# Performance work log

Measured on AMD Instinct MI355X. Metric: run time of the kernel, lower is better.

The kernel has to match this reference:

```python
import jax, jax.numpy as jnp
import numpy as np

D_IN = 2048
NUM_HEADS = 32
NUM_KV = 8
HEAD_DIM = 64
V_HEAD_DIM = 64
SEQ = 2048
BATCH = 1
EPS = 1e-6
NEG = -1e30


def setup_inputs() -> dict:
    key = jax.random.key(0)
    ks = jax.random.split(key, 10)
    x = jax.random.normal(ks[0], (BATCH, SEQ, D_IN), dtype=jnp.float32)
    # causal mask: True = masked out (upper triangle above diagonal)
    mask = jnp.triu(jnp.ones((SEQ, SEQ), dtype=jnp.bool_), k=1)
    # RoPE tables
    inv_freq = 1.0 / (10000.0 ** (jnp.arange(0, HEAD_DIM, 2, dtype=jnp.float32) / HEAD_DIM))
    t = jnp.arange(SEQ, dtype=jnp.float32)
    freqs = jnp.outer(t, inv_freq)  # (S, hd/2)
    emb = jnp.concatenate([freqs, freqs], axis=-1)  # (S, hd)
    cos = jnp.cos(emb)
    sin = jnp.sin(emb)
    scale = 0.02
    wq = jax.random.normal(ks[1], (D_IN, NUM_HEADS * HEAD_DIM), dtype=jnp.float32) * scale
    wk = jax.random.normal(ks[2], (D_IN, NUM_KV * HEAD_DIM), dtype=jnp.float32) * scale
    wv = jax.random.normal(ks[3], (D_IN, NUM_KV * V_HEAD_DIM), dtype=jnp.float32) * scale
    wo = jax.random.normal(ks[4], (NUM_HEADS * V_HEAD_DIM, D_IN), dtype=jnp.float32) * scale
    q_norm_w = jnp.ones((HEAD_DIM,), dtype=jnp.float32)
    k_norm_w = jnp.ones((HEAD_DIM,), dtype=jnp.float32)
    sink = jax.random.normal(ks[5], (NUM_HEADS,), dtype=jnp.float32) * 0.02
    return {"x": x, "mask": mask, "cos": cos, "sin": sin, "wq": wq, "wk": wk,
            "wv": wv, "wo": wo, "q_norm_w": q_norm_w, "k_norm_w": k_norm_w, "sink": sink}


def _rmsnorm(x, w):
    var = jnp.mean(jnp.square(x), axis=-1, keepdims=True)
    return x * jax.lax.rsqrt(var + EPS) * w


def _rope(x, cos, sin):
    # x: (b, h, s, d); cos/sin: (s, d)
    d = x.shape[-1]
    x1, x2 = x[..., : d // 2], x[..., d // 2:]
    rot = jnp.concatenate([-x2, x1], axis=-1)
    return x * cos[None, None] + rot * sin[None, None]


def reference(x, mask, cos, sin, wq, wk, wv, wo, q_norm_w, k_norm_w, sink):
    b, s, _ = x.shape
    rep = NUM_HEADS // NUM_KV
    q = (x @ wq).reshape(b, s, NUM_HEADS, HEAD_DIM).transpose(0, 2, 1, 3)
    k = (x @ wk).reshape(b, s, NUM_KV, HEAD_DIM).transpose(0, 2, 1, 3)
    v = (x @ wv).reshape(b, s, NUM_KV, V_HEAD_DIM).transpose(0, 2, 1, 3)
    q = _rope(_rmsnorm(q, q_norm_w), cos, sin)
    k = _rope(_rmsnorm(k, k_norm_w), cos, sin)
    k = jnp.repeat(k, rep, axis=1)  # (b, H, s, hd)
    v = jnp.repeat(v, rep, axis=1)  # (b, H, s, vd)
    scores = jnp.einsum('bhqd,bhkd->bhqk', q, k) * (HEAD_DIM ** -0.5)
    scores = jnp.where(mask[:s, :s], NEG, scores)
    # append learnable sink logit per head
    sink_col = jnp.broadcast_to(sink.reshape(1, NUM_HEADS, 1, 1), (b, NUM_HEADS, s, 1))
    scores = jnp.concatenate([scores, sink_col], axis=-1)
    weights = jax.nn.softmax(scores, axis=-1)[..., :-1]  # drop sink column
    out = jnp.einsum('bhqk,bhkd->bhqd', weights, v)
    out = out.transpose(0, 2, 1, 3).reshape(b, s, NUM_HEADS * V_HEAD_DIM)
    return out @ wo
```

## Files before the change

### kernel.cpp

```cpp
#include <hip/hip_runtime.h>

typedef unsigned short u16;
typedef __bf16 bf16;
typedef float f32x4 __attribute__((ext_vector_type(4)));
typedef bf16 bf16x8 __attribute__((ext_vector_type(8)));
typedef short s16x4 __attribute__((ext_vector_type(4)));
typedef u16 u16x4 __attribute__((ext_vector_type(4)));
typedef u16 u16x8 __attribute__((ext_vector_type(8)));

#define SEQ 2048
#define LOG2E 1.4426950408889634f

__device__ __forceinline__ u16 f2bf(float f) {
    return __builtin_bit_cast(u16, (bf16)f);
}
__device__ __forceinline__ float bf2f(u16 u) {
    unsigned int w = ((unsigned int)u) << 16;
    return __builtin_bit_cast(float, w);
}

__global__ __launch_bounds__(256) void cast_bf16_k(const float* __restrict__ in,
                                                   u16* __restrict__ out, int n4) {
    int i = blockIdx.x * 256 + threadIdx.x;
    int stride = gridDim.x * 256;
    for (; i < n4; i += stride) {
        float4 v = reinterpret_cast<const float4*>(in)[i];
        u16x4 o;
        o[0] = f2bf(v.x); o[1] = f2bf(v.y); o[2] = f2bf(v.z); o[3] = f2bf(v.w);
        reinterpret_cast<u16x4*>(out)[i] = o;
    }
}

__global__ __launch_bounds__(256) void transpose_all_k(const float* __restrict__ wq,
                                                       const float* __restrict__ wk,
                                                       const float* __restrict__ wv,
                                                       const float* __restrict__ wo,
                                                       u16* __restrict__ wqkvt,
                                                       u16* __restrict__ wot) {
    __shared__ float t[64][65];
    int b = blockIdx.x;
    const float* src;
    u16* dst;
    int C, bx, by;
    if (b < 1024)      { src = wq; dst = wqkvt;                         C = 2048; bx = b & 31; by = b >> 5; }
    else if (b < 1280) { b -= 1024; src = wk; dst = wqkvt + (size_t)2048 * 2048; C = 512;  bx = b & 7;  by = b >> 3; }
    else if (b < 1536) { b -= 1280; src = wv; dst = wqkvt + (size_t)2560 * 2048; C = 512;  bx = b & 7;  by = b >> 3; }
    else               { b -= 1536; src = wo; dst = wot;                C = 2048; bx = b & 31; by = b >> 5; }
    int c0 = bx * 64, r0 = by * 64;
    int tx = threadIdx.x & 63, ty = threadIdx.x >> 6;
#pragma unroll
    for (int i = 0; i < 16; ++i) {
        int r = ty + i * 4;
        t[r][tx] = src[(size_t)(r0 + r) * C + c0 + tx];
    }
    __syncthreads();
#pragma unroll
    for (int i = 0; i < 16; ++i) {
        int c = ty + i * 4;
        dst[(size_t)(c0 + c) * 2048 + r0 + tx] = f2bf(t[tx][c]);
    }
}

__global__ __launch_bounds__(256) void gemm_bt_dbuf_k(const u16* __restrict__ A,
                                                      const u16* __restrict__ Bt,
                                                      u16* __restrict__ Cp,
                                                      int M, int N, int K) {
    __shared__ __align__(16) u16 As[2][128 * 32];
    __shared__ __align__(16) u16 Bs[2][128 * 32];
    int tid = threadIdx.x;
    int wave = tid >> 6, lane = tid & 63;

    unsigned nx = gridDim.x, ny = gridDim.y;
    unsigned nwg = nx * ny * gridDim.z;
    unsigned id = blockIdx.x + nx * (blockIdx.y + ny * blockIdx.z);
    unsigned qq = nwg >> 3;
    unsigned swz = (id & 7) * qq + (id >> 3);
    unsigned bxw = swz % nx;
    unsigned rem = swz / nx;
    unsigned byw = rem % ny;
    unsigned bzw = rem / ny;
    int bm = byw * 128, bn = bxw * 128;
    int z = bzw;

    int kslice = K / gridDim.z;
    int kt0 = z * kslice, ktend = kt0 + kslice;
    int wm = (wave >> 1) * 64, wn = (wave & 1) * 64;
    int g = lane >> 4, cidx = lane & 15;
    f32x4 acc[4][4] = {};

    int srow = lane >> 2;
    int skol = ((lane & 3) ^ ((srow >> 1) & 3)) * 8;
    int sl8 = (g ^ ((cidx >> 1) & 3)) * 8;

#define STAGE(buf, kt)                                                                \
    {                                                                                 \
        _Pragma("unroll")                                                             \
        for (int j = 0; j < 2; ++j) {                                                 \
            const u16* gpa = A + (size_t)(bm + (wave * 2 + j) * 16 + srow) * K + (kt) + skol; \
            __builtin_amdgcn_global_load_lds(                                         \
                (__attribute__((address_space(1))) void*)gpa,                         \
                (__attribute__((address_space(3))) void*)&As[buf][(wave * 2 + j) * 512], \
                16, 0, 0);                                                            \
        }                                                                             \
        _Pragma("unroll")                                                             \
        for (int j = 0; j < 2; ++j) {                                                 \
            const u16* gpb = Bt + (size_t)(bn + (wave * 2 + j) * 16 + srow) * K + (kt) + skol; \
            __builtin_amdgcn_global_load_lds(                                         \
                (__attribute__((address_space(1))) void*)gpb,                         \
                (__attribute__((address_space(3))) void*)&Bs[buf][(wave * 2 + j) * 512], \
                16, 0, 0);                                                            \
        }                                                                             \
    }

    STAGE(0, kt0);
    asm volatile("s_waitcnt vmcnt(0)" ::: "memory");
    __syncthreads();

    int cur = 0;
#pragma unroll 1
    for (int kt = kt0; kt < ktend; kt += 32) {
        if (kt + 32 < ktend) STAGE(cur ^ 1, kt + 32);

        bf16x8 af[4], bfr[4];
#pragma unroll
        for (int mi = 0; mi < 4; ++mi)
            af[mi] = *reinterpret_cast<const bf16x8*>(&As[cur][(wm + mi * 16 + cidx) * 32 + sl8]);
#pragma unroll
        for (int ni = 0; ni < 4; ++ni)
            bfr[ni] = *reinterpret_cast<const bf16x8*>(&Bs[cur][(wn + ni * 16 + cidx) * 32 + sl8]);
#pragma unroll
        for (int mi = 0; mi < 4; ++mi)
#pragma unroll
            for (int ni = 0; ni < 4; ++ni)
                acc[mi][ni] = __builtin_amdgcn_mfma_f32_16x16x32_bf16(af[mi], bfr[ni], acc[mi][ni], 0, 0, 0);

        asm volatile("s_waitcnt vmcnt(0)" ::: "memory");
        __syncthreads();
        cur ^= 1;
    }
#undef STAGE

    u16* cbase = Cp + (size_t)z * M * N;
#pragma unroll
    for (int mi = 0; mi < 4; ++mi) {
#pragma unroll
        for (int r = 0; r < 4; ++r) {
            int row = bm + wm + mi * 16 + g * 4 + r;
            u16* cp = cbase + (size_t)row * N + bn + wn + cidx;
#pragma unroll
            for (int ni = 0; ni < 4; ++ni)
                cp[ni * 16] = f2bf(acc[mi][ni][r]);
        }
    }
}

__global__ __launch_bounds__(256) void sum2_f32_k(const u16* __restrict__ a,
                                                  const u16* __restrict__ b,
                                                  float* __restrict__ out, int n8) {
    int i = blockIdx.x * 256 + threadIdx.x;
    if (i >= n8) return;
    u16x8 va = reinterpret_cast<const u16x8*>(a)[i];
    u16x8 vb = reinterpret_cast<const u16x8*>(b)[i];
    f32x4 lo, hi;
#pragma unroll
    for (int j = 0; j < 4; ++j) {
        lo[j] = bf2f(va[j]) + bf2f(vb[j]);
        hi[j] = bf2f(va[4 + j]) + bf2f(vb[4 + j]);
    }
    reinterpret_cast<f32x4*>(out)[i * 2] = lo;
    reinterpret_cast<f32x4*>(out)[i * 2 + 1] = hi;
}

__global__ __launch_bounds__(256) void norm_rope_k(const u16* __restrict__ p0,
                                                   const u16* __restrict__ p1,
                                                   const float* __restrict__ cosb,
                                                   const float* __restrict__ sinb,
                                                   const float* __restrict__ qw,
                                                   const float* __restrict__ kw,
                                                   u16* __restrict__ qn,
                                                   u16* __restrict__ kfrag) {
    int idx = blockIdx.x * 4 + (threadIdx.x >> 6);
    int lane = threadIdx.x & 63;
    int s = idx / 40, hh = idx - s * 40;
    size_t off = (hh < 32) ? ((size_t)s * 3072 + hh * 64 + lane)
                           : ((size_t)s * 3072 + 2048 + (hh - 32) * 64 + lane);
    float val = bf2f(p0[off]) + bf2f(p1[off]);
    float ss = val * val;
#pragma unroll
    for (int mm = 32; mm; mm >>= 1) ss += __shfl_xor(ss, mm);
    float w = (hh < 32) ? qw[lane] : kw[lane];
    float xn = val * rsqrtf(ss * (1.f / 64.f) + 1e-6f) * w;
    float part = __shfl_xor(xn, 32);
    float rot = (lane < 32) ? -part : part;
    float o = xn * cosb[s * 64 + lane] + rot * sinb[s * 64 + lane];
    if (hh < 32) {
        qn[(size_t)s * 2048 + hh * 64 + lane] = f2bf(o * (0.125f * LOG2E));
    } else {
        int h8 = hh - 32;
        int k32 = s & 31;
        int p32 = ((k32 >> 2) & 1) * 16 + ((k32 >> 3) << 2) + (k32 & 3);
        int p = (s & ~31) + p32;
        kfrag[(((size_t)h8 * 128 + (p >> 4)) << 10) + (lane >> 3) * 128 + (p & 15) * 8 + (lane & 7)] = f2bf(o);
    }
}

__global__ __launch_bounds__(256) void v_frag_k(const u16* __restrict__ p0,
                                                const u16* __restrict__ p1,
                                                u16* __restrict__ vfrag) {
    __shared__ float t[64][65];
    int s0 = blockIdx.x * 64;
    int h = blockIdx.y;
    int tx = threadIdx.x & 63, ty = threadIdx.x >> 6;
#pragma unroll
    for (int i = 0; i < 16; ++i) {
        int r = ty + i * 4;
        size_t off = (size_t)(s0 + r) * 3072 + 2560 + h * 64 + tx;
        t[r][tx] = bf2f(p0[off]) + bf2f(p1[off]);
    }
    __syncthreads();
    int dt = threadIdx.x >> 6, g = (threadIdx.x >> 4) & 3, cc = threadIdx.x & 15;
#pragma unroll
    for (int kb = 0; kb < 2; ++kb) {
        u16x8 o;
#pragma unroll
        for (int i = 0; i < 8; ++i) o[i] = f2bf(t[kb * 32 + g * 8 + i][dt * 16 + cc]);
        *reinterpret_cast<u16x8*>(
            &vfrag[((size_t)h * 64 + (s0 >> 5) + kb) * 2048 + dt * 512 + (size_t)(threadIdx.x & 63) * 8]) = o;
    }
}

__global__ __launch_bounds__(64, 3) void attn_k(const u16* __restrict__ qn,
                                                const u16* __restrict__ kfrag,
                                                const u16* __restrict__ vfrag,
                                                u16* __restrict__ obuf,
                                                float* __restrict__ lbuf) {
    int h = blockIdx.x;
    int kvh = h >> 2;
    int lane = threadIdx.x;
    int item = 159 - blockIdx.y;
    int t, w;
    if (item < 16)      { t = item;                    w = 0; }
    else if (item < 48) { t = 16 + ((item - 16) >> 1); w = (item - 16) & 1; }
    else if (item < 96) { int r = item - 48; int q = r / 3; t = 32 + q; w = r - 3 * q; }
    else                { t = 48 + ((item - 96) >> 2); w = (item - 96) & 3; }

    int qA0 = t * 32;
    int qB0 = qA0 + 16;
    int kv0 = w * 512;
    int nkA = qA0 + 16, nkB = qB0 + 16;
    int kvend = (kv0 + 512 < nkB) ? (kv0 + 512) : nkB;

    int g = lane >> 4, cc = lane & 15;
    int qrowA = qA0 + cc, qrowB = qB0 + cc;

    const size_t qoffA = (size_t)qrowA * 2048 + h * 64;
    const size_t qoffB = (size_t)qrowB * 2048 + h * 64;
    bf16x8 qa0 = *reinterpret_cast<const bf16x8*>(&qn[qoffA + g * 8]);
    bf16x8 qa1 = *reinterpret_cast<const bf16x8*>(&qn[qoffA + 32 + g * 8]);
    bf16x8 qb0 = *reinterpret_cast<const bf16x8*>(&qn[qoffB + g * 8]);
    bf16x8 qb1 = *reinterpret_cast<const bf16x8*>(&qn[qoffB + 32 + g * 8]);

    float lA = 0.f, lB = 0.f;
    f32x4 oA[4] = {}, oB[4] = {};

    const u16* kbase = kfrag + (((size_t)kvh * 128) << 10) + lane * 8;
    const u16* vbase = vfrag + (size_t)kvh * 64 * 2048 + lane * 8;

#pragma unroll 1
    for (; kv0 < kvend; kv0 += 64) {
        bf16x8 kf0[4], kf1[4], vv[2][4];
#pragma unroll
        for (int sub = 0; sub < 4; ++sub) {
            const u16* kp = kbase + (size_t)((kv0 >> 4) + sub) * 1024;
            kf0[sub] = *reinterpret_cast<const bf16x8*>(kp);
            kf1[sub] = *reinterpret_cast<const bf16x8*>(kp + 512);
        }
#pragma unroll
        for (int sp = 0; sp < 2; ++sp)
#pragma unroll
            for (int dt = 0; dt < 4; ++dt)
                vv[sp][dt] = *reinterpret_cast<const bf16x8*>(
                    vbase + (size_t)((kv0 >> 5) + sp) * 2048 + dt * 512);

        bool doA = kv0 < nkA;

        if (doA) {
            f32x4 st[4];
            __builtin_amdgcn_s_setprio(1);
#pragma unroll
            for (int sub = 0; sub < 4; ++sub) {
                st[sub] = __builtin_amdgcn_mfma_f32_16x16x32_bf16(kf0[sub], qa0, (f32x4){0.f, 0.f, 0.f, 0.f}, 0, 0, 0);
                st[sub] = __builtin_amdgcn_mfma_f32_16x16x32_bf16(kf1[sub], qa1, st[sub], 0, 0, 0);
            }
            __builtin_amdgcn_s_setprio(0);
            if (kv0 + 64 > qA0) {
#pragma unroll
                for (int sub = 0; sub < 4; ++sub)
#pragma unroll
                    for (int r = 0; r < 4; ++r) {
                        int key = kv0 + (sub >> 1) * 32 + g * 8 + (sub & 1) * 4 + r;
                        if (key > qrowA) st[sub][r] = -1e30f;
                    }
            }
            u16x8 pb[2];
            float rs = 0.f;
#pragma unroll
            for (int sub = 0; sub < 4; ++sub)
#pragma unroll
                for (int r = 0; r < 4; ++r) {
                    float e = __builtin_amdgcn_exp2f(st[sub][r]);
                    rs += e;
                    pb[sub >> 1][(sub & 1) * 4 + r] = f2bf(e);
                }
            lA += rs;
            __builtin_amdgcn_s_setprio(1);
#pragma unroll
            for (int sp = 0; sp < 2; ++sp) {
                bf16x8 pbb = __builtin_bit_cast(bf16x8, pb[sp]);
#pragma unroll
                for (int dt = 0; dt < 4; ++dt)
                    oA[dt] = __builtin_amdgcn_mfma_f32_16x16x32_bf16(vv[sp][dt], pbb, oA[dt], 0, 0, 0);
            }
            __builtin_amdgcn_s_setprio(0);
        }

        {
            f32x4 st[4];
            __builtin_amdgcn_s_setprio(1);
#pragma unroll
            for (int sub = 0; sub < 4; ++sub) {
                st[sub] = __builtin_amdgcn_mfma_f32_16x16x32_bf16(kf0[sub], qb0, (f32x4){0.f, 0.f, 0.f, 0.f}, 0, 0, 0);
                st[sub] = __builtin_amdgcn_mfma_f32_16x16x32_bf16(kf1[sub], qb1, st[sub], 0, 0, 0);
            }
            __builtin_amdgcn_s_setprio(0);
            if (kv0 + 64 > qB0) {
#pragma unroll
                for (int sub = 0; sub < 4; ++sub)
#pragma unroll
                    for (int r = 0; r < 4; ++r) {
                        int key = kv0 + (sub >> 1) * 32 + g * 8 + (sub & 1) * 4 + r;
                        if (key > qrowB) st[sub][r] = -1e30f;
                    }
            }
            u16x8 pb[2];
            float rs = 0.f;
#pragma unroll
            for (int sub = 0; sub < 4; ++sub)
#pragma unroll
                for (int r = 0; r < 4; ++r) {
                    float e = __builtin_amdgcn_exp2f(st[sub][r]);
                    rs += e;
                    pb[sub >> 1][(sub & 1) * 4 + r] = f2bf(e);
                }
            lB += rs;
            __builtin_amdgcn_s_setprio(1);
#pragma unroll
            for (int sp = 0; sp < 2; ++sp) {
                bf16x8 pbb = __builtin_bit_cast(bf16x8, pb[sp]);
#pragma unroll
                for (int dt = 0; dt < 4; ++dt)
                    oB[dt] = __builtin_amdgcn_mfma_f32_16x16x32_bf16(vv[sp][dt], pbb, oB[dt], 0, 0, 0);
            }
            __builtin_amdgcn_s_setprio(0);
        }
    }

    lA += __shfl_xor(lA, 16);
    lA += __shfl_xor(lA, 32);
    lB += __shfl_xor(lB, 16);
    lB += __shfl_xor(lB, 32);
    size_t slotA = ((size_t)h * 160 + item) * 2;
    if (lane < 16) {
        lbuf[slotA * 16 + cc] = lA;
        lbuf[(slotA + 1) * 16 + cc] = lB;
    }
    u16* spA = obuf + slotA * 1024;
    u16* spB = obuf + (slotA + 1) * 1024;
#pragma unroll
    for (int dt = 0; dt < 4; ++dt) {
        u16x4 ovA, ovB;
#pragma unroll
        for (int r = 0; r < 4; ++r) {
            ovA[r] = f2bf(oA[dt][r]);
            ovB[r] = f2bf(oB[dt][r]);
        }
        *reinterpret_cast<u16x4*>(&spA[cc * 64 + dt * 16 + g * 4]) = ovA;
        *reinterpret_cast<u16x4*>(&spB[cc * 64 + dt * 16 + g * 4]) = ovB;
    }
}

__global__ __launch_bounds__(256) void merge_k(const u16* __restrict__ obuf,
                                               const float* __restrict__ lbuf,
                                               const float* __restrict__ sink,
                                               u16* __restrict__ attnb) {
    int row = blockIdx.x;
    int c = row >> 4, cc = row & 15;
    int t2 = c >> 1, half = c & 1;
    int nw = (t2 >> 4) + 1;
    int jb = (t2 < 16) ? t2
           : (t2 < 32) ? 16 + ((t2 - 16) << 1)
           : (t2 < 48) ? 48 + 3 * (t2 - 32)
                       : 96 + ((t2 - 48) << 2);
    int t = threadIdx.x;
    int h = t >> 3, col0 = (t & 7) * 8;

    float acc[8] = {};
    float lsum = __builtin_amdgcn_exp2f(sink[h] * LOG2E);
#pragma unroll 1
    for (int w = 0; w < nw; ++w) {
        size_t slot = ((size_t)h * 160 + jb + w) * 2 + half;
        lsum += lbuf[slot * 16 + cc];
        u16x8 v = *reinterpret_cast<const u16x8*>(&obuf[slot * 1024 + cc * 64 + col0]);
#pragma unroll
        for (int i = 0; i < 8; ++i) acc[i] += bf2f(v[i]);
    }
    float inv = 1.f / lsum;
    u16x8 ob;
#pragma unroll
    for (int i = 0; i < 8; ++i) ob[i] = f2bf(acc[i] * inv);
    *reinterpret_cast<u16x8*>(&attnb[(size_t)row * 2048 + h * 64 + col0]) = ob;
}

extern "C" void kernel_launch(void* const* d_in, const int* in_sizes, int n_in,
                              void* d_out, int out_size, void* d_ws, size_t ws_size,
                              hipStream_t stream) {
    const float* x    = (const float*)d_in[0];
    const float* cosb = (const float*)d_in[2];
    const float* sinb = (const float*)d_in[3];
    const float* wq   = (const float*)d_in[4];
    const float* wk   = (const float*)d_in[5];
    const float* wv   = (const float*)d_in[6];
    const float* wo   = (const float*)d_in[7];
    const float* qw   = (const float*)d_in[8];
    const float* kw   = (const float*)d_in[9];
    const float* sink = (const float*)d_in[10];
    float* out = (float*)d_out;

    char* ws = (char*)d_ws;
    size_t off = 0;
    auto alloc = [&](size_t bytes) {
        char* p = ws + off;
        off += (bytes + 255) & ~(size_t)255;
        return p;
    };
    u16*   xb    = (u16*)alloc((size_t)2048 * 2048 * 2);
    u16*   wqkvt = (u16*)alloc((size_t)3072 * 2048 * 2);
    u16*   wot   = (u16*)alloc((size_t)2048 * 2048 * 2);
    u16*   p0    = (u16*)alloc((size_t)2048 * 3072 * 2);
    u16*   p1    = (u16*)alloc((size_t)2048 * 3072 * 2);
    u16*   qnb   = (u16*)alloc((size_t)2048 * 2048 * 2);
    u16*   kfrag = (u16*)alloc((size_t)8 * 128 * 1024 * 2);
    u16*   vfrag = (u16*)alloc((size_t)8 * 64 * 2048 * 2);
    float* lbuf  = (float*)alloc((size_t)32 * 320 * 16 * 4);
    u16*   attnb = xb;
    u16*   obuf  = p0;
    u16*   o2p   = p0;

    cast_bf16_k<<<2048, 256, 0, stream>>>(x, xb, 2048 * 2048 / 4);
    transpose_all_k<<<2560, 256, 0, stream>>>(wq, wk, wv, wo, wqkvt, wot);

    gemm_bt_dbuf_k<<<dim3(24, 16, 2), 256, 0, stream>>>(xb, wqkvt, p0, 2048, 3072, 2048);
    norm_rope_k<<<20480, 256, 0, stream>>>(p0, p1, cosb, sinb, qw, kw, qnb, kfrag);
    v_frag_k<<<dim3(32, 8), 256, 0, stream>>>(p0, p1, vfrag);

    attn_k<<<dim3(32, 160), 64, 0, stream>>>(qnb, kfrag, vfrag, obuf, lbuf);
    merge_k<<<2048, 256, 0, stream>>>(obuf, lbuf, sink, attnb);

    gemm_bt_dbuf_k<<<dim3(16, 16, 2), 256, 0, stream>>>(attnb, wot, o2p, 2048, 2048, 2048);
    sum2_f32_k<<<2048, 256, 0, stream>>>(o2p, o2p + (size_t)2048 * 2048, out, 2048 * 2048 / 8);
}
```

Baseline: 140.7 us.

## Merge prep and post-GEMM kernels; restructure attention loop and raise occupancy

Combines the x cast and weight transposes into one prep kernel, and the norm/RoPE and V-fragment kernels into one post-GEMM kernel, removing two launches. In the attention kernel, V loads are deferred until after both score blocks are computed and the PV MFMAs for both query halves are interleaved. Launch bounds go from 3 to 4 waves per SIMD. The higher occupancy target lowers the per-thread register budget and could cause spills, and the fused kernels mix dissimilar block workloads.

```diff
diff --git a/kernel.cpp b/kernel.cpp
--- a/kernel.cpp
+++ b/kernel.cpp
@@ -19,33 +19,35 @@
     return __builtin_bit_cast(float, w);
 }
 
-__global__ __launch_bounds__(256) void cast_bf16_k(const float* __restrict__ in,
-                                                   u16* __restrict__ out, int n4) {
-    int i = blockIdx.x * 256 + threadIdx.x;
-    int stride = gridDim.x * 256;
-    for (; i < n4; i += stride) {
-        float4 v = reinterpret_cast<const float4*>(in)[i];
-        u16x4 o;
-        o[0] = f2bf(v.x); o[1] = f2bf(v.y); o[2] = f2bf(v.z); o[3] = f2bf(v.w);
-        reinterpret_cast<u16x4*>(out)[i] = o;
-    }
-}
-
-__global__ __launch_bounds__(256) void transpose_all_k(const float* __restrict__ wq,
-                                                       const float* __restrict__ wk,
-                                                       const float* __restrict__ wv,
-                                                       const float* __restrict__ wo,
-                                                       u16* __restrict__ wqkvt,
-                                                       u16* __restrict__ wot) {
+__global__ __launch_bounds__(256) void prep_k(const float* __restrict__ x,
+                                              const float* __restrict__ wq,
+                                              const float* __restrict__ wk,
+                                              const float* __restrict__ wv,
+                                              const float* __restrict__ wo,
+                                              u16* __restrict__ xb,
+                                              u16* __restrict__ wqkvt,
+                                              u16* __restrict__ wot) {
     __shared__ float t[64][65];
     int b = blockIdx.x;
+    if (b < 2048) {
+        int i = b * 256 + threadIdx.x;
+#pragma unroll
+        for (int it = 0; it < 2; ++it, i += 524288) {
+            float4 v = reinterpret_cast<const float4*>(x)[i];
+            u16x4 o;
+            o[0] = f2bf(v.x); o[1] = f2bf(v.y); o[2] = f2bf(v.z); o[3] = f2bf(v.w);
+            reinterpret_cast<u16x4*>(xb)[i] = o;
+        }
+        return;
+    }
+    b -= 2048;
     const float* src;
     u16* dst;
     int C, bx, by;
-    if (b < 1024)      { src = wq; dst = wqkvt;                         C = 2048; bx = b & 31; by = b >> 5; }
-    else if (b < 1280) { b -= 1024; src = wk; dst = wqkvt + (size_t)2048 * 2048; C = 512;  bx = b & 7;  by = b >> 3; }
-    else if (b < 1536) { b -= 1280; src = wv; dst = wqkvt + (size_t)2560 * 2048; C = 512;  bx = b & 7;  by = b >> 3; }
-    else               { b -= 1536; src = wo; dst = wot;                C = 2048; bx = b & 31; by = b >> 5; }
+    if (b < 1024)      { src = wq; dst = wqkvt;                          C = 2048; bx = b & 31; by = b >> 5; }
+    else if (b < 1280) { b -= 1024; src = wk; dst = wqkvt + (size_t)2048 * 2048; C = 512; bx = b & 7; by = b >> 3; }
+    else if (b < 1536) { b -= 1280; src = wv; dst = wqkvt + (size_t)2560 * 2048; C = 512; bx = b & 7; by = b >> 3; }
+    else               { b -= 1536; src = wo; dst = wot;                 C = 2048; bx = b & 31; by = b >> 5; }
     int c0 = bx * 64, r0 = by * 64;
     int tx = threadIdx.x & 63, ty = threadIdx.x >> 6;
 #pragma unroll
@@ -171,45 +173,45 @@
     reinterpret_cast<f32x4*>(out)[i * 2 + 1] = hi;
 }
 
-__global__ __launch_bounds__(256) void norm_rope_k(const u16* __restrict__ p0,
-                                                   const u16* __restrict__ p1,
-                                                   const float* __restrict__ cosb,
-                                                   const float* __restrict__ sinb,
-                                                   const float* __restrict__ qw,
-                                                   const float* __restrict__ kw,
-                                                   u16* __restrict__ qn,
-                                                   u16* __restrict__ kfrag) {
-    int idx = blockIdx.x * 4 + (threadIdx.x >> 6);
-    int lane = threadIdx.x & 63;
-    int s = idx / 40, hh = idx - s * 40;
-    size_t off = (hh < 32) ? ((size_t)s * 3072 + hh * 64 + lane)
-                           : ((size_t)s * 3072 + 2048 + (hh - 32) * 64 + lane);
-    float val = bf2f(p0[off]) + bf2f(p1[off]);
-    float ss = val * val;
-#pragma unroll
-    for (int mm = 32; mm; mm >>= 1) ss += __shfl_xor(ss, mm);
-    float w = (hh < 32) ? qw[lane] : kw[lane];
-    float xn = val * rsqrtf(ss * (1.f / 64.f) + 1e-6f) * w;
-    float part = __shfl_xor(xn, 32);
-    float rot = (lane < 32) ? -part : part;
-    float o = xn * cosb[s * 64 + lane] + rot * sinb[s * 64 + lane];
-    if (hh < 32) {
-        qn[(size_t)s * 2048 + hh * 64 + lane] = f2bf(o * (0.125f * LOG2E));
-    } else {
-        int h8 = hh - 32;
-        int k32 = s & 31;
-        int p32 = ((k32 >> 2) & 1) * 16 + ((k32 >> 3) << 2) + (k32 & 3);
-        int p = (s & ~31) + p32;
-        kfrag[(((size_t)h8 * 128 + (p >> 4)) << 10) + (lane >> 3) * 128 + (p & 15) * 8 + (lane & 7)] = f2bf(o);
-    }
-}
-
-__global__ __launch_bounds__(256) void v_frag_k(const u16* __restrict__ p0,
-                                                const u16* __restrict__ p1,
-                                                u16* __restrict__ vfrag) {
+__global__ __launch_bounds__(256) void postgemm_k(const u16* __restrict__ p0,
+                                                  const u16* __restrict__ p1,
+                                                  const float* __restrict__ cosb,
+                                                  const float* __restrict__ sinb,
+                                                  const float* __restrict__ qw,
+                                                  const float* __restrict__ kw,
+                                                  u16* __restrict__ qn,
+                                                  u16* __restrict__ kfrag,
+                                                  u16* __restrict__ vfrag) {
     __shared__ float t[64][65];
-    int s0 = blockIdx.x * 64;
-    int h = blockIdx.y;
+    int b = blockIdx.x;
+    if (b < 20480) {
+        int idx = b * 4 + (threadIdx.x >> 6);
+        int lane = threadIdx.x & 63;
+        int s = idx / 40, hh = idx - s * 40;
+        size_t off = (hh < 32) ? ((size_t)s * 3072 + hh * 64 + lane)
+                               : ((size_t)s * 3072 + 2048 + (hh - 32) * 64 + lane);
+        float val = bf2f(p0[off]) + bf2f(p1[off]);
+        float ss = val * val;
+#pragma unroll
+        for (int mm = 32; mm; mm >>= 1) ss += __shfl_xor(ss, mm);
+        float w = (hh < 32) ? qw[lane] : kw[lane];
+        float xn = val * rsqrtf(ss * (1.f / 64.f) + 1e-6f) * w;
+        float part = __shfl_xor(xn, 32);
+        float rot = (lane < 32) ? -part : part;
+        float o = xn * cosb[s * 64 + lane] + rot * sinb[s * 64 + lane];
+        if (hh < 32) {
+            qn[(size_t)s * 2048 + hh * 64 + lane] = f2bf(o * (0.125f * LOG2E));
+        } else {
+            int h8 = hh - 32;
+            int k32 = s & 31;
+            int p32 = ((k32 >> 2) & 1) * 16 + ((k32 >> 3) << 2) + (k32 & 3);
+            int p = (s & ~31) + p32;
+            kfrag[(((size_t)h8 * 128 + (p >> 4)) << 10) + (lane >> 3) * 128 + (p & 15) * 8 + (lane & 7)] = f2bf(o);
+        }
+        return;
+    }
+    int vb = b - 20480;
+    int s0 = (vb & 31) * 64, h = vb >> 5;
     int tx = threadIdx.x & 63, ty = threadIdx.x >> 6;
 #pragma unroll
     for (int i = 0; i < 16; ++i) {
@@ -229,7 +231,7 @@
     }
 }
 
-__global__ __launch_bounds__(64, 3) void attn_k(const u16* __restrict__ qn,
+__global__ __launch_bounds__(64, 4) void attn_k(const u16* __restrict__ qn,
                                                 const u16* __restrict__ kfrag,
                                                 const u16* __restrict__ vfrag,
                                                 u16* __restrict__ obuf,
@@ -268,63 +270,46 @@
 
 #pragma unroll 1
     for (; kv0 < kvend; kv0 += 64) {
-        bf16x8 kf0[4], kf1[4], vv[2][4];
-#pragma unroll
-        for (int sub = 0; sub < 4; ++sub) {
-            const u16* kp = kbase + (size_t)((kv0 >> 4) + sub) * 1024;
-            kf0[sub] = *reinterpret_cast<const bf16x8*>(kp);
-            kf1[sub] = *reinterpret_cast<const bf16x8*>(kp + 512);
-        }
-#pragma unroll
-        for (int sp = 0; sp < 2; ++sp)
-#pragma unroll
-            for (int dt = 0; dt < 4; ++dt)
-                vv[sp][dt] = *reinterpret_cast<const bf16x8*>(
-                    vbase + (size_t)((kv0 >> 5) + sp) * 2048 + dt * 512);
-
         bool doA = kv0 < nkA;
-
-        if (doA) {
-            f32x4 st[4];
-            __builtin_amdgcn_s_setprio(1);
+        u16x8 pbA[2], pbB[2];
+
+        {
+            bf16x8 kf0[4], kf1[4];
 #pragma unroll
             for (int sub = 0; sub < 4; ++sub) {
-                st[sub] = __builtin_amdgcn_mfma_f32_16x16x32_bf16(kf0[sub], qa0, (f32x4){0.f, 0.f, 0.f, 0.f}, 0, 0, 0);
-                st[sub] = __builtin_amdgcn_mfma_f32_16x16x32_bf16(kf1[sub], qa1, st[sub], 0, 0, 0);
+                const u16* kp = kbase + (size_t)((kv0 >> 4) + sub) * 1024;
+                kf0[sub] = *reinterpret_cast<const bf16x8*>(kp);
+                kf1[sub] = *reinterpret_cast<const bf16x8*>(kp + 512);
             }
-            __builtin_amdgcn_s_setprio(0);
-            if (kv0 + 64 > qA0) {
+            if (doA) {
+                f32x4 st[4];
+                __builtin_amdgcn_s_setprio(1);
+#pragma unroll
+                for (int sub = 0; sub < 4; ++sub) {
+                    st[sub] = __builtin_amdgcn_mfma_f32_16x16x32_bf16(kf0[sub], qa0, (f32x4){0.f, 0.f, 0.f, 0.f}, 0, 0, 0);
+                    st[sub] = __builtin_amdgcn_mfma_f32_16x16x32_bf16(kf1[sub], qa1, st[sub], 0, 0, 0);
+                }
+                __builtin_amdgcn_s_setprio(0);
+                if (kv0 + 64 > qA0) {
+#pragma unroll
+                    for (int sub = 0; sub < 4; ++sub)
+#pragma unroll
+                        for (int r = 0; r < 4; ++r) {
+                            int key = kv0 + (sub >> 1) * 32 + g * 8 + (sub & 1) * 4 + r;
+                            if (key > qrowA) st[sub][r] = -1e30f;
+                        }
+                }
+                float rs = 0.f;
 #pragma unroll
                 for (int sub = 0; sub < 4; ++sub)
 #pragma unroll
                     for (int r = 0; r < 4; ++r) {
-                        int key = kv0 + (sub >> 1) * 32 + g * 8 + (sub & 1) * 4 + r;
-                        if (key > qrowA) st[sub][r] = -1e30f;
+                        float e = __builtin_amdgcn_exp2f(st[sub][r]);
+                        rs += e;
+                        pbA[sub >> 1][(sub & 1) * 4 + r] = f2bf(e);
                     }
+                lA += rs;
             }
-            u16x8 pb[2];
-            float rs = 0.f;
-#pragma unroll
-            for (int sub = 0; sub < 4; ++sub)
-#pragma unroll
-                for (int r = 0; r < 4; ++r) {
-                    float e = __builtin_amdgcn_exp2f(st[sub][r]);
-                    rs += e;
-                    pb[sub >> 1][(sub & 1) * 4 + r] = f2bf(e);
-                }
-            lA += rs;
-            __builtin_amdgcn_s_setprio(1);
-#pragma unroll
-            for (int sp = 0; sp < 2; ++sp) {
-                bf16x8 pbb = __builtin_bit_cast(bf16x8, pb[sp]);
-#pragma unroll
-                for (int dt = 0; dt < 4; ++dt)
-                    oA[dt] = __builtin_amdgcn_mfma_f32_16x16x32_bf16(vv[sp][dt], pbb, oA[dt], 0, 0, 0);
-            }
-            __builtin_amdgcn_s_setprio(0);
-        }
-
-        {
             f32x4 st[4];
             __builtin_amdgcn_s_setprio(1);
 #pragma unroll
@@ -342,7 +327,6 @@
                         if (key > qrowB) st[sub][r] = -1e30f;
                     }
             }
-            u16x8 pb[2];
             float rs = 0.f;
 #pragma unroll
             for (int sub = 0; sub < 4; ++sub)
@@ -350,19 +334,31 @@
                 for (int r = 0; r < 4; ++r) {
                     float e = __builtin_amdgcn_exp2f(st[sub][r]);
                     rs += e;
-                    pb[sub >> 1][(sub & 1) * 4 + r] = f2bf(e);
+                    pbB[sub >> 1][(sub & 1) * 4 + r] = f2bf(e);
                 }
             lB += rs;
-            __builtin_amdgcn_s_setprio(1);
-#pragma unroll
-            for (int sp = 0; sp < 2; ++sp) {
-                bf16x8 pbb = __builtin_bit_cast(bf16x8, pb[sp]);
-#pragma unroll
-                for (int dt = 0; dt < 4; ++dt)
-                    oB[dt] = __builtin_amdgcn_mfma_f32_16x16x32_bf16(vv[sp][dt], pbb, oB[dt], 0, 0, 0);
+        }
+
+        bf16x8 vv[2][4];
+#pragma unroll
+        for (int sp = 0; sp < 2; ++sp)
+#pragma unroll
+            for (int dt = 0; dt < 4; ++dt)
+                vv[sp][dt] = *reinterpret_cast<const bf16x8*>(
+                    vbase + (size_t)((kv0 >> 5) + sp) * 2048 + dt * 512);
+
+        __builtin_amdgcn_s_setprio(1);
+#pragma unroll
+        for (int sp = 0; sp < 2; ++sp) {
+            bf16x8 pa = __builtin_bit_cast(bf16x8, pbA[sp]);
+            bf16x8 pb = __builtin_bit_cast(bf16x8, pbB[sp]);
+#pragma unroll
+            for (int dt = 0; dt < 4; ++dt) {
+                if (doA) oA[dt] = __builtin_amdgcn_mfma_f32_16x16x32_bf16(vv[sp][dt], pa, oA[dt], 0, 0, 0);
+                oB[dt] = __builtin_amdgcn_mfma_f32_16x16x32_bf16(vv[sp][dt], pb, oB[dt], 0, 0, 0);
             }
-            __builtin_amdgcn_s_setprio(0);
-        }
+        }
+        __builtin_amdgcn_s_setprio(0);
     }
 
     lA += __shfl_xor(lA, 16);
@@ -456,12 +452,10 @@
     u16*   obuf  = p0;
     u16*   o2p   = p0;
 
-    cast_bf16_k<<<2048, 256, 0, stream>>>(x, xb, 2048 * 2048 / 4);
-    transpose_all_k<<<2560, 256, 0, stream>>>(wq, wk, wv, wo, wqkvt, wot);
+    prep_k<<<4608, 256, 0, stream>>>(x, wq, wk, wv, wo, xb, wqkvt, wot);
 
     gemm_bt_dbuf_k<<<dim3(24, 16, 2), 256, 0, stream>>>(xb, wqkvt, p0, 2048, 3072, 2048);
-    norm_rope_k<<<20480, 256, 0, stream>>>(p0, p1, cosb, sinb, qw, kw, qnb, kfrag);
-    v_frag_k<<<dim3(32, 8), 256, 0, stream>>>(p0, p1, vfrag);
+    postgemm_k<<<20736, 256, 0, stream>>>(p0, p1, cosb, sinb, qw, kw, qnb, kfrag, vfrag);
 
     attn_k<<<dim3(32, 160), 64, 0, stream>>>(qnb, kfrag, vfrag, obuf, lbuf);
     merge_k<<<2048, 256, 0, stream>>>(obuf, lbuf, sink, attnb);
```

After: 138.6 us. No clear change (-1.5%).
